# Performance work log

Hardware: AMD Instinct MI355X
Metric: run time of the kernel (lower is better)

The kernel has to match this reference:

```python
import jax, jax.numpy as jnp
import numpy as np

H, D = 8, 16
F = H * D              # hidden_dim = 128
L = 2                  # num HGT layers
NS = [50000, 20000, 10000]                     # gene, disease, drug node counts
EDGE_META = [(0, 0), (0, 1), (2, 0), (2, 1)]   # (src_type, dst_type) per edge type
ES = [300000, 150000, 100000, 50000]
OFFS = [0, NS[0], NS[0] + NS[1], NS[0] + NS[1] + NS[2]]
NTOT = OFFS[-1]
R, T = len(EDGE_META), len(NS)
SQRT_D = float(np.sqrt(D))


def setup_inputs() -> dict:
    key = jax.random.key(0)
    ks = jax.random.split(key, 32)
    inp = {}
    inp["x_gene"] = jax.random.normal(ks[0], (NS[0], F), jnp.float32)
    inp["x_disease"] = jax.random.normal(ks[1], (NS[1], F), jnp.float32)
    inp["x_drug"] = jax.random.normal(ks[2], (NS[2], F), jnp.float32)
    inp["Wkqv"] = 0.05 * jax.random.normal(ks[3], (L, T, F, 3 * F), jnp.float32)
    inp["bkqv"] = jnp.zeros((L, T, 3 * F), jnp.float32)
    inp["Ak"] = 0.1 * jax.random.normal(ks[4], (L, R, H, D, D), jnp.float32)
    inp["Av"] = 0.1 * jax.random.normal(ks[5], (L, R, H, D, D), jnp.float32)
    inp["prel"] = jnp.ones((L, R, H), jnp.float32)   # PyG inits p_rel to ones
    inp["Wout"] = 0.05 * jax.random.normal(ks[6], (L, T, F, F), jnp.float32)
    inp["bout"] = jnp.zeros((L, T, F), jnp.float32)
    inp["skip"] = jnp.ones((L, T), jnp.float32)      # PyG inits skip to 1
    names = ["ei_gg", "ei_gd", "ei_rg", "ei_rd"]
    for i, (name, (st, dt), E) in enumerate(zip(names, EDGE_META, ES)):
        src = jax.random.randint(ks[10 + 2 * i], (E,), 0, NS[st], dtype=jnp.int32)
        dst = jax.random.randint(ks[11 + 2 * i], (E,), 0, NS[dt], dtype=jnp.int32)
        inp[name] = jnp.stack([src, dst])
    return inp


def _hgt_layer(xs, eis, Wkqv_l, bkqv_l, Ak_l, Av_l, prel_l, Wout_l, bout_l, skip_l):
    """One PyG-style HGTConv layer over the heterogeneous graph."""
    kqv = [x @ Wkqv_l[t] + bkqv_l[t] for t, x in enumerate(xs)]
    k = [a[:, :F].reshape(-1, H, D) for a in kqv]
    q = [a[:, F:2 * F].reshape(-1, H, D) for a in kqv]
    v = [a[:, 2 * F:].reshape(-1, H, D) for a in kqv]

    alphas, dsts, ves = [], [], []
    for r, (st, dt) in enumerate(EDGE_META):
        src, dst = eis[r][0], eis[r][1]
        # relation-specific per-head transforms applied on source node set
        k_r = jnp.einsum('nhd,hde->nhe', k[st], Ak_l[r])
        v_r = jnp.einsum('nhd,hde->nhe', v[st], Av_l[r])
        ke = k_r[src]                      # [E, H, D]
        ve = v_r[src]                      # [E, H, D]
        qe = q[dt][dst]                    # [E, H, D]
        a = (qe * ke).sum(-1) * prel_l[r] / SQRT_D   # [E, H]
        alphas.append(a)
        dsts.append(dst + OFFS[dt])
        ves.append(ve)
    alpha = jnp.concatenate(alphas, 0)     # [Etot, H]
    dstg = jnp.concatenate(dsts, 0)        # [Etot]
    ve = jnp.concatenate(ves, 0)           # [Etot, H, D]

    # segment softmax over all incoming edges per destination node
    amax = jax.ops.segment_max(alpha, dstg, num_segments=NTOT)
    ex = jnp.exp(alpha - amax[dstg])
    denom = jax.ops.segment_sum(ex, dstg, num_segments=NTOT)
    w = ex / denom[dstg]
    out = jax.ops.segment_sum(ve * w[..., None], dstg, num_segments=NTOT)
    out = out.reshape(NTOT, F)

    new_xs = []
    for t, x in enumerate(xs):
        o_t = out[OFFS[t]:OFFS[t + 1]]
        o = jax.nn.gelu(o_t, approximate=False) @ Wout_l[t] + bout_l[t]
        a_s = jax.nn.sigmoid(skip_l[t])
        new_xs.append(a_s * o + (1.0 - a_s) * x)
    return new_xs


def reference(x_gene, x_disease, x_drug, Wkqv, bkqv, Ak, Av, prel, Wout, bout,
              skip, ei_gg, ei_gd, ei_rg, ei_rd):
    xs = [x_gene, x_disease, x_drug]
    eis = [ei_gg, ei_gd, ei_rg, ei_rd]
    for l in range(L):
        new = _hgt_layer(xs, eis, Wkqv[l], bkqv[l], Ak[l], Av[l], prel[l],
                         Wout[l], bout[l], skip[l])
        # encoder: dropout(relu(conv_out)) + residual; dropout = identity (eval)
        xs = [jax.nn.relu(n) + x for n, x in zip(new, xs)]
    return tuple(xs)
```

## Files before the change

### kernel.cpp

```cpp
#include <hip/hip_runtime.h>


#define NTOT  80000
#define ETOT  600000
#define NSRC  120000

typedef unsigned short u16;
typedef unsigned int   u32;
typedef __attribute__((ext_vector_type(8))) short short8;
typedef __attribute__((ext_vector_type(4))) float f32x4;

__device__ __forceinline__ float bf2f(u16 u){
  union { u32 i; float f; } v; v.i = ((u32)u) << 16; return v.f;
}
__device__ __forceinline__ u16 f2bf(float f){
  union { float f; u32 i; } v; v.f = f;
  u32 x = v.i;
  return (u16)((x + 0x7fffu + ((x >> 16) & 1u)) >> 16);
}
__device__ __forceinline__ void unp4(uint4 a, float* o){
  union { u32 i; float f; } t;
  t.i = a.x << 16;        o[0]=t.f;  t.i = a.x & 0xffff0000u; o[1]=t.f;
  t.i = a.y << 16;        o[2]=t.f;  t.i = a.y & 0xffff0000u; o[3]=t.f;
  t.i = a.z << 16;        o[4]=t.f;  t.i = a.z & 0xffff0000u; o[5]=t.f;
  t.i = a.w << 16;        o[6]=t.f;  t.i = a.w & 0xffff0000u; o[7]=t.f;
}
__device__ __forceinline__ void load16bf(const u16* p, float* o){
  unp4(*(const uint4*)p, o); unp4(*(const uint4*)(p + 8), o + 8);
}


__global__ __launch_bounds__(256) void copy_init(
    const float* __restrict__ xg, const float* __restrict__ xd,
    const float* __restrict__ xr, float* __restrict__ X, u16* __restrict__ Xbf)
{
  int i = blockIdx.x * 256 + threadIdx.x;
  if (i >= 2560000) return;
  const float* src; int off;
  if (i < 1600000)      { src = xg; off = i; }
  else if (i < 2240000) { src = xd; off = i - 1600000; }
  else                  { src = xr; off = i - 2240000; }
  float4 v = ((const float4*)src)[off];
  ((float4*)X)[i] = v;
  uint2 b;
  b.x = (u32)f2bf(v.x) | ((u32)f2bf(v.y) << 16);
  b.y = (u32)f2bf(v.z) | ((u32)f2bf(v.w) << 16);
  ((uint2*)Xbf)[i] = b;
}

__global__ __launch_bounds__(256) void zero_cc(int* __restrict__ cnt, int* __restrict__ cur){
  int i = blockIdx.x * 256 + threadIdx.x;
  if (i < NTOT){ cnt[i] = 0; cur[i] = 0; }
}


__global__ __launch_bounds__(256) void count_all(
    const int* __restrict__ e0, const int* __restrict__ e1,
    const int* __restrict__ e2, const int* __restrict__ e3,
    int* __restrict__ cnt)
{
  int e = blockIdx.x * 256 + threadIdx.x;
  if (e >= ETOT) return;
  const int* ei; int E, loc, offd;
  if (e < 300000)      { ei = e0; E = 300000; loc = e;          offd = 0; }
  else if (e < 450000) { ei = e1; E = 150000; loc = e - 300000; offd = 50000; }
  else if (e < 550000) { ei = e2; E = 100000; loc = e - 450000; offd = 0; }
  else                 { ei = e3; E = 50000;  loc = e - 550000; offd = 50000; }
  atomicAdd(&cnt[offd + ei[E + loc]], 1);
}

__global__ __launch_bounds__(256) void scan_partial(const int* __restrict__ cnt,
                             int* __restrict__ rowp, int* __restrict__ bsum){
  __shared__ int s[256];
  int tid = threadIdx.x;
  int i = blockIdx.x * 256 + tid;
  int v = (i < NTOT) ? cnt[i] : 0;
  s[tid] = v; __syncthreads();
  for (int off = 1; off < 256; off <<= 1){
    int t = (tid >= off) ? s[tid - off] : 0;
    __syncthreads();
    s[tid] += t;
    __syncthreads();
  }
  if (i < NTOT) rowp[i] = s[tid] - v;
  if (tid == 255) bsum[blockIdx.x] = s[255];
}

__global__ __launch_bounds__(256) void scan_block(int* __restrict__ bsum, int nb){
  __shared__ int b[512];
  __shared__ int p[256];
  int tid = threadIdx.x;
  b[tid]       = (tid < nb)       ? bsum[tid]       : 0;
  b[tid + 256] = (tid + 256 < nb) ? bsum[tid + 256] : 0;
  __syncthreads();
  int pv = b[2*tid] + b[2*tid + 1];
  p[tid] = pv; __syncthreads();
  for (int off = 1; off < 256; off <<= 1){
    int t = (tid >= off) ? p[tid - off] : 0;
    __syncthreads();
    p[tid] += t;
    __syncthreads();
  }
  int excl = p[tid] - pv;
  int e0 = excl, e1 = excl + b[2*tid];
  __syncthreads();
  if (2*tid < nb)   bsum[2*tid]     = e0;
  if (2*tid+1 < nb) bsum[2*tid + 1] = e1;
}

__global__ __launch_bounds__(256) void scan_add(int* __restrict__ rowp, const int* __restrict__ bsum){
  int i = blockIdx.x * 256 + threadIdx.x;
  if (i < NTOT) rowp[i] += bsum[i >> 8];
}

__global__ __launch_bounds__(256) void scatter_all(
    const int* __restrict__ e0, const int* __restrict__ e1,
    const int* __restrict__ e2, const int* __restrict__ e3,
    const int* __restrict__ rowp, int* __restrict__ cur,
    int* __restrict__ elist)
{
  int e = blockIdx.x * 256 + threadIdx.x;
  if (e >= ETOT) return;
  const int* ei; int E, loc, offd, rnoff, rel;
  if (e < 300000)      { ei = e0; E = 300000; loc = e;          offd = 0;     rnoff = 0;      rel = 0; }
  else if (e < 450000) { ei = e1; E = 150000; loc = e - 300000; offd = 50000; rnoff = 50000;  rel = 1; }
  else if (e < 550000) { ei = e2; E = 100000; loc = e - 450000; offd = 0;     rnoff = 100000; rel = 2; }
  else                 { ei = e3; E = 50000;  loc = e - 550000; offd = 50000; rnoff = 110000; rel = 3; }
  int src = ei[loc], dst = ei[E + loc];
  int dstg = offd + dst;
  int pos = atomicAdd(&cur[dstg], 1);
  elist[rowp[dstg] + pos] = ((rnoff + src) << 2) | rel;
}


__global__ __launch_bounds__(256) void build_wefft(
    const float* __restrict__ Wkqv, const float* __restrict__ Ak,
    const float* __restrict__ Av, u16* __restrict__ WeffT)
{
  int i = blockIdx.x * 256 + threadIdx.x;
  if (i >= 8*32768) return;
  int lr = i >> 15, rem = i & 32767, n = rem >> 7, k = rem & 127;
  int l = lr >> 2, r = lr & 3;
  int st = (r >= 2) ? 2 : 0;
  const float* W = Wkqv + (size_t)(l*3 + st) * 49152;
  float acc = 0.f;
  if (n < 128){
    int h = n >> 4, e = n & 15;
    const float* Am = Ak + (size_t)(l*4 + r) * 2048 + h*256;
#pragma unroll
    for (int d = 0; d < 16; d++) acc += W[k*384 + h*16 + d] * Am[d*16 + e];
  } else {
    int n2 = n - 128, h = n2 >> 4, e = n2 & 15;
    const float* Am = Av + (size_t)(l*4 + r) * 2048 + h*256;
#pragma unroll
    for (int d = 0; d < 16; d++) acc += W[k*384 + 256 + h*16 + d] * Am[d*16 + e];
  }
  WeffT[i] = f2bf(acc);
}

__global__ __launch_bounds__(256) void build_beff(
    const float* __restrict__ bkqv, const float* __restrict__ Ak,
    const float* __restrict__ Av, float* __restrict__ beff)
{
  int lr = blockIdx.x;
  int l = lr >> 2, r = lr & 3;
  int st = (r >= 2) ? 2 : 0;
  int j = threadIdx.x;
  const float* b = bkqv + (size_t)(l*3 + st) * 384;
  float acc = 0.f;
  if (j < 128){
    int h = j >> 4, e = j & 15;
    const float* Am = Ak + (size_t)(l*4 + r) * 2048 + h*256;
#pragma unroll
    for (int d = 0; d < 16; d++) acc += b[h*16 + d] * Am[d*16 + e];
  } else {
    int j2 = j - 128, h = j2 >> 4, e = j2 & 15;
    const float* Am = Av + (size_t)(l*4 + r) * 2048 + h*256;
#pragma unroll
    for (int d = 0; d < 16; d++) acc += b[256 + h*16 + d] * Am[d*16 + e];
  }
  beff[lr * 256 + j] = acc;
}


__global__ __launch_bounds__(256) void conv_w(
    const float* __restrict__ Wkqv, const float* __restrict__ Wout,
    u16* __restrict__ WqT, u16* __restrict__ WoutT)
{
  int i = blockIdx.x * 256 + threadIdx.x;
  if (i >= 2*6*16384) return;
  if (i < 6*16384){
    int lt = i >> 14, rem = i & 16383, n = rem >> 7, k = rem & 127;
    WqT[i] = f2bf(Wkqv[(size_t)lt*49152 + k*384 + 128 + n]);
  } else {
    int j = i - 6*16384;
    int lt = j >> 14, rem = j & 16383, n = rem >> 7, k = rem & 127;
    WoutT[j] = f2bf(Wout[(size_t)lt*16384 + k*128 + n]);
  }
}


__device__ __forceinline__ void stage_bt(const u16* __restrict__ src, u16* BTl){
  int tid = threadIdx.x;
  const uint4* g = (const uint4*)src;
  uint4 tmp[8];
#pragma unroll
  for (int i = 0; i < 8; i++) tmp[i] = g[tid + i*256];
#pragma unroll
  for (int i = 0; i < 8; i++){
    int L = (tid + i*256) * 16;
    int Ls = L ^ (((L >> 8) & 7) << 4);
    *(uint4*)((char*)BTl + Ls) = tmp[i];
  }
  __syncthreads();
}

__device__ __forceinline__ void gemm_core(
    const u16* __restrict__ A, const u16* BTl, int M, int bm,
    f32x4 acc[8][2])
{
  int tid = threadIdx.x;
  int lane = tid & 63, w = tid >> 6;
  int quad = lane >> 4, lm = lane & 15;
  short8 af[2][4];
#pragma unroll
  for (int mf = 0; mf < 2; mf++){
    int row = bm + w*32 + mf*16 + lm;
    if (row < M){
      const u16* ap = A + (size_t)row*128 + quad*8;
#pragma unroll
      for (int c = 0; c < 4; c++) af[mf][c] = *(const short8*)(ap + c*32);
    } else {
      short8 z = {0,0,0,0,0,0,0,0};
#pragma unroll
      for (int c = 0; c < 4; c++) af[mf][c] = z;
    }
  }
#pragma unroll
  for (int nt = 0; nt < 8; nt++)
#pragma unroll
    for (int mf = 0; mf < 2; mf++) acc[nt][mf] = (f32x4){0.f,0.f,0.f,0.f};
#pragma unroll
  for (int nt = 0; nt < 8; nt++){
    int rowb = nt*16 + lm;
    int base = rowb*256 + quad*16;
    int sw = (rowb & 7) << 4;
#pragma unroll
    for (int c = 0; c < 4; c++){
      short8 bf = *(const short8*)((const char*)BTl + ((base + c*64) ^ sw));
      acc[nt][0] = __builtin_amdgcn_mfma_f32_16x16x32_bf16(af[0][c], bf, acc[nt][0], 0, 0, 0);
      acc[nt][1] = __builtin_amdgcn_mfma_f32_16x16x32_bf16(af[1][c], bf, acc[nt][1], 0, 0, 0);
    }
  }
}

__global__ __launch_bounds__(256) void mfma_gemm_q(
    const u16* __restrict__ Xbf, const u16* __restrict__ WqTl,
    const float* __restrict__ bl, u16* __restrict__ qg)
{
  __shared__ u16 BTl[16384];
  int by = blockIdx.x;
  int t, bm, M, roff;
  if (by < 391)      { t = 0; bm = by*128;        M = 50000; roff = 0; }
  else if (by < 548) { t = 1; bm = (by-391)*128;  M = 20000; roff = 50000; }
  else               { t = 2; bm = (by-548)*128;  M = 10000; roff = 70000; }
  stage_bt(WqTl + (size_t)t*16384, BTl);
  const u16* A = Xbf + (size_t)roff*128;
  const float* bias = bl + (size_t)t*384 + 128;
  u16* C = qg + (size_t)roff*128;
  f32x4 acc[8][2];
  gemm_core(A, BTl, M, bm, acc);
  int lane = threadIdx.x & 63, w = threadIdx.x >> 6;
  int quad = lane >> 4, lm = lane & 15;
#pragma unroll
  for (int nt = 0; nt < 8; nt++){
    int col = nt*16 + lm;
    float bb = bias[col];
#pragma unroll
    for (int mf = 0; mf < 2; mf++)
#pragma unroll
      for (int i = 0; i < 4; i++){
        int r = bm + w*32 + mf*16 + quad*4 + i;
        if (r < M) C[(size_t)r*128 + col] = f2bf(acc[nt][mf][i] + bb);
      }
  }
}

__global__ __launch_bounds__(256) void mfma_gemm_kv(
    const u16* __restrict__ Xbf, const u16* __restrict__ WeffTl,
    const float* __restrict__ beffl, u16* __restrict__ kv)
{
  __shared__ u16 BTl[16384];
  int by = blockIdx.y;
  int r, bm, M, soff, ooff;
  if (by < 391)      { r = 0; bm = by*128;        M = 50000; soff = 0;     ooff = 0; }
  else if (by < 782) { r = 1; bm = (by-391)*128;  M = 50000; soff = 0;     ooff = 50000; }
  else if (by < 861) { r = 2; bm = (by-782)*128;  M = 10000; soff = 70000; ooff = 100000; }
  else               { r = 3; bm = (by-861)*128;  M = 10000; soff = 70000; ooff = 110000; }
  int bn = blockIdx.x * 128;
  stage_bt(WeffTl + (size_t)r*32768 + (size_t)bn*128, BTl);
  const u16* A = Xbf + (size_t)soff*128;
  const float* bias = beffl + (size_t)r*256;
  u16* C = kv + (size_t)ooff*256;
  f32x4 acc[8][2];
  gemm_core(A, BTl, M, bm, acc);
  int lane = threadIdx.x & 63, w = threadIdx.x >> 6;
  int quad = lane >> 4, lm = lane & 15;
#pragma unroll
  for (int nt = 0; nt < 8; nt++){
    int col = bn + nt*16 + lm;
    float bb = bias[col];
#pragma unroll
    for (int mf = 0; mf < 2; mf++)
#pragma unroll
      for (int i = 0; i < 4; i++){
        int r2 = bm + w*32 + mf*16 + quad*4 + i;
        if (r2 < M) C[(size_t)r2*256 + col] = f2bf(acc[nt][mf][i] + bb);
      }
  }
}

__global__ __launch_bounds__(256) void mfma_gemm_out(
    const u16* __restrict__ Gall, const u16* __restrict__ WoutTl,
    const float* __restrict__ bl, const float* __restrict__ skipl,
    float* __restrict__ Xall, u16* __restrict__ Xbfall)
{
  __shared__ u16 BTl[16384];
  int by = blockIdx.x;
  int t, bm, M, roff;
  if (by < 391)      { t = 0; bm = by*128;        M = 50000; roff = 0; }
  else if (by < 548) { t = 1; bm = (by-391)*128;  M = 20000; roff = 50000; }
  else               { t = 2; bm = (by-548)*128;  M = 10000; roff = 70000; }
  stage_bt(WoutTl + (size_t)t*16384, BTl);
  const u16* A = Gall + (size_t)roff*128;
  const float* bias = bl + (size_t)t*128;
  float* X = Xall + (size_t)roff*128;
  u16* Xb = Xbfall + (size_t)roff*128;
  f32x4 acc[8][2];
  gemm_core(A, BTl, M, bm, acc);
  float a_s = 1.f / (1.f + expf(-skipl[t]));
  float b_s = 1.f - a_s;
  int lane = threadIdx.x & 63, w = threadIdx.x >> 6;
  int quad = lane >> 4, lm = lane & 15;
#pragma unroll
  for (int nt = 0; nt < 8; nt++){
    int col = nt*16 + lm;
    float bb = bias[col];
#pragma unroll
    for (int mf = 0; mf < 2; mf++)
#pragma unroll
      for (int i = 0; i < 4; i++){
        int r = bm + w*32 + mf*16 + quad*4 + i;
        if (r < M){
          float* xp = X + (size_t)r*128 + col;
          float x = *xp;
          float o = acc[nt][mf][i] + bb;
          float xn = fmaxf(a_s*o + b_s*x, 0.f) + x;
          *xp = xn;
          Xb[(size_t)r*128 + col] = f2bf(xn);
        }
      }
  }
}


__global__ __launch_bounds__(256) void attn_kernel(
    u16* __restrict__ qg,
    const u16* __restrict__ kv,
    const float* __restrict__ prel,
    const int* __restrict__ rowp, const int* __restrict__ cnt,
    const int* __restrict__ elist)
{
  int gid = blockIdx.x * 256 + threadIdx.x;
  int n = gid >> 4;
  if (n >= NTOT) return;
  int lane = threadIdx.x & 63;
  int sub = (lane >> 3) & 1;
  int h = lane & 7;
  float sc0 = prel[0*8+h]*0.25f, sc1 = prel[1*8+h]*0.25f,
        sc2 = prel[2*8+h]*0.25f, sc3 = prel[3*8+h]*0.25f;
  float q[16];
  load16bf(qg + (size_t)n * 128 + h*16, q);
  float acc[16] = {};
  float dsum = 0.f;
  int start = rowp[n], c = cnt[n];

  auto edge = [&](int ev, uint4 ka, uint4 kb, uint4 va, uint4 vb){
    float ke[16], ve[16];
    unp4(ka, ke); unp4(kb, ke + 8);
    unp4(va, ve); unp4(vb, ve + 8);
    float a = 0.f;
#pragma unroll
    for (int d = 0; d < 16; d++) a += q[d] * ke[d];
    int r = ev & 3;
    float s = (r == 0) ? sc0 : (r == 1) ? sc1 : (r == 2) ? sc2 : sc3;
    float ex = expf(a * s);
    dsum += ex;
#pragma unroll
    for (int d = 0; d < 16; d++) acc[d] += ex * ve[d];
  };

  int idx = sub;
#pragma unroll 1
  for (; idx + 6 < c; idx += 8){
    int e0 = elist[start + idx + 0], e1 = elist[start + idx + 2],
        e2 = elist[start + idx + 4], e3 = elist[start + idx + 6];
    const u16* p0 = kv + (size_t)(e0 >> 2) * 256 + h*16;
    const u16* p1 = kv + (size_t)(e1 >> 2) * 256 + h*16;
    const u16* p2 = kv + (size_t)(e2 >> 2) * 256 + h*16;
    const u16* p3 = kv + (size_t)(e3 >> 2) * 256 + h*16;
    uint4 k0a = *(const uint4*)p0,         k0b = *(const uint4*)(p0 + 8);
    uint4 k1a = *(const uint4*)p1,         k1b = *(const uint4*)(p1 + 8);
    uint4 k2a = *(const uint4*)p2,         k2b = *(const uint4*)(p2 + 8);
    uint4 k3a = *(const uint4*)p3,         k3b = *(const uint4*)(p3 + 8);
    uint4 v0a = *(const uint4*)(p0 + 128), v0b = *(const uint4*)(p0 + 136);
    uint4 v1a = *(const uint4*)(p1 + 128), v1b = *(const uint4*)(p1 + 136);
    uint4 v2a = *(const uint4*)(p2 + 128), v2b = *(const uint4*)(p2 + 136);
    uint4 v3a = *(const uint4*)(p3 + 128), v3b = *(const uint4*)(p3 + 136);
    edge(e0, k0a, k0b, v0a, v0b);
    edge(e1, k1a, k1b, v1a, v1b);
    edge(e2, k2a, k2b, v2a, v2b);
    edge(e3, k3a, k3b, v3a, v3b);
  }
#pragma unroll 1
  for (; idx < c; idx += 2){
    int ev = elist[start + idx];
    const u16* p = kv + (size_t)(ev >> 2) * 256 + h*16;
    uint4 ka = *(const uint4*)p,         kb = *(const uint4*)(p + 8);
    uint4 va = *(const uint4*)(p + 128), vb = *(const uint4*)(p + 136);
    edge(ev, ka, kb, va, vb);
  }

  dsum += __shfl_xor(dsum, 8);
#pragma unroll
  for (int d = 0; d < 16; d++) acc[d] += __shfl_xor(acc[d], 8);

  if (sub == 0){
    float inv = (c > 0) ? 1.f / dsum : 0.f;
    u16 o[16];
#pragma unroll
    for (int d = 0; d < 16; d++){
      float x = acc[d] * inv;
      o[d] = f2bf(0.5f * x * (1.f + erff(x * 0.70710678118654752f)));
    }
    uint4 p0, p1;
    p0.x = o[0]|(o[1]<<16);   p0.y = o[2]|(o[3]<<16);
    p0.z = o[4]|(o[5]<<16);   p0.w = o[6]|(o[7]<<16);
    p1.x = o[8]|(o[9]<<16);   p1.y = o[10]|(o[11]<<16);
    p1.z = o[12]|(o[13]<<16); p1.w = o[14]|(o[15]<<16);
    u16* op = qg + (size_t)n * 128 + h*16;
    *(uint4*)op = p0; *(uint4*)(op + 8) = p1;
  }
}


extern "C" void kernel_launch(void* const* d_in, const int* in_sizes, int n_in,
                              void* d_out, int out_size, void* d_ws, size_t ws_size,
                              hipStream_t stream)
{
  const float* xg   = (const float*)d_in[0];
  const float* xd   = (const float*)d_in[1];
  const float* xr_  = (const float*)d_in[2];
  const float* Wkqv = (const float*)d_in[3];
  const float* bkqv = (const float*)d_in[4];
  const float* Ak   = (const float*)d_in[5];
  const float* Av   = (const float*)d_in[6];
  const float* prel = (const float*)d_in[7];
  const float* Wout = (const float*)d_in[8];
  const float* bout = (const float*)d_in[9];
  const float* skip = (const float*)d_in[10];
  const int* ei[4] = {(const int*)d_in[11], (const int*)d_in[12],
                      (const int*)d_in[13], (const int*)d_in[14]};

  float* X = (float*)d_out;

  char* p = (char*)d_ws;
  auto alloc = [&](size_t b)->void*{ void* r = (void*)p; p += (b + 255) & ~(size_t)255; return r; };
  int*   cnt   = (int*)  alloc((size_t)NTOT * 4);
  int*   rowp  = (int*)  alloc((size_t)NTOT * 4);
  int*   cur   = (int*)  alloc((size_t)NTOT * 4);
  int*   bsum  = (int*)  alloc(512 * 4);
  int*   elist = (int*)  alloc((size_t)ETOT * 4);
  float* beff  = (float*)alloc((size_t)8 * 256 * 4);
  u16*   qg    = (u16*)  alloc((size_t)NTOT * 128 * 2);
  u16*   kv    = (u16*)  alloc((size_t)NSRC * 256 * 2);
  u16*   Xbf   = (u16*)  alloc((size_t)NTOT * 128 * 2);
  u16*   WqT   = (u16*)  alloc((size_t)6 * 16384 * 2);
  u16*   WeffT = (u16*)  alloc((size_t)8 * 32768 * 2);
  u16*   WoutT = (u16*)  alloc((size_t)6 * 16384 * 2);
  (void)ws_size; (void)in_sizes; (void)n_in; (void)out_size;

  copy_init<<<10000, 256, 0, stream>>>(xg, xd, xr_, X, Xbf);
  zero_cc<<<313, 256, 0, stream>>>(cnt, cur);

  count_all<<<(ETOT+255)/256, 256, 0, stream>>>(ei[0], ei[1], ei[2], ei[3], cnt);
  scan_partial<<<313, 256, 0, stream>>>(cnt, rowp, bsum);
  scan_block<<<1, 256, 0, stream>>>(bsum, 313);
  scan_add<<<313, 256, 0, stream>>>(rowp, bsum);
  scatter_all<<<(ETOT+255)/256, 256, 0, stream>>>(ei[0], ei[1], ei[2], ei[3], rowp, cur, elist);

  build_wefft<<<1024, 256, 0, stream>>>(Wkqv, Ak, Av, WeffT);
  build_beff<<<8, 256, 0, stream>>>(bkqv, Ak, Av, beff);
  conv_w<<<768, 256, 0, stream>>>(Wkqv, Wout, WqT, WoutT);

  for (int l = 0; l < 2; l++){
    mfma_gemm_q<<<627, 256, 0, stream>>>(
        Xbf, WqT + (size_t)l*3*16384, bkqv + (size_t)l*3*384, qg);
    mfma_gemm_kv<<<dim3(2, 940), 256, 0, stream>>>(
        Xbf, WeffT + (size_t)l*4*32768, beff + (size_t)l*4*256, kv);
    attn_kernel<<<5000, 256, 0, stream>>>(qg, kv, prel + l*32, rowp, cnt, elist);
    mfma_gemm_out<<<627, 256, 0, stream>>>(
        qg, WoutT + (size_t)l*3*16384, bout + (size_t)l*3*128, skip + l*3, X, Xbf);
  }
}
```

Before: 467.8 us.

## Merge Q and KV GEMMs into one launch, halve M-tile, fuse setup kernels

Combines the Q projection GEMM and the relation-specific K/V GEMM into a single kernel dispatched over a flat block index. The per-block M tile drops from 128 to 64 rows, so each wave handles one 16-row fragment, and the output GEMM gets the same tile size. The init/zero kernels and the three weight-preparation kernels are each merged into one launch. The aim is to cut launch count and improve occupancy and tail balance. The cost is twice as many blocks, each restaging the 32KB B tile into LDS, so there is less B reuse per staging.

```diff
diff --git a/kernel.cpp b/kernel.cpp
--- a/kernel.cpp
+++ b/kernel.cpp
@@ -30,27 +30,27 @@
 }
 
 
-__global__ __launch_bounds__(256) void copy_init(
+__global__ __launch_bounds__(256) void init_all(
     const float* __restrict__ xg, const float* __restrict__ xd,
-    const float* __restrict__ xr, float* __restrict__ X, u16* __restrict__ Xbf)
+    const float* __restrict__ xr, float* __restrict__ X, u16* __restrict__ Xbf,
+    int* __restrict__ cnt, int* __restrict__ cur)
 {
   int i = blockIdx.x * 256 + threadIdx.x;
-  if (i >= 2560000) return;
-  const float* src; int off;
-  if (i < 1600000)      { src = xg; off = i; }
-  else if (i < 2240000) { src = xd; off = i - 1600000; }
-  else                  { src = xr; off = i - 2240000; }
-  float4 v = ((const float4*)src)[off];
-  ((float4*)X)[i] = v;
-  uint2 b;
-  b.x = (u32)f2bf(v.x) | ((u32)f2bf(v.y) << 16);
-  b.y = (u32)f2bf(v.z) | ((u32)f2bf(v.w) << 16);
-  ((uint2*)Xbf)[i] = b;
-}
-
-__global__ __launch_bounds__(256) void zero_cc(int* __restrict__ cnt, int* __restrict__ cur){
-  int i = blockIdx.x * 256 + threadIdx.x;
-  if (i < NTOT){ cnt[i] = 0; cur[i] = 0; }
+  if (i < 2560000){
+    const float* src; int off;
+    if (i < 1600000)      { src = xg; off = i; }
+    else if (i < 2240000) { src = xd; off = i - 1600000; }
+    else                  { src = xr; off = i - 2240000; }
+    float4 v = ((const float4*)src)[off];
+    ((float4*)X)[i] = v;
+    uint2 b;
+    b.x = (u32)f2bf(v.x) | ((u32)f2bf(v.y) << 16);
+    b.y = (u32)f2bf(v.z) | ((u32)f2bf(v.w) << 16);
+    ((uint2*)Xbf)[i] = b;
+  } else {
+    int j = i - 2560000;
+    if (j < NTOT){ cnt[j] = 0; cur[j] = 0; }
+  }
 }
 
 
@@ -133,70 +133,65 @@
 }
 
 
-__global__ __launch_bounds__(256) void build_wefft(
-    const float* __restrict__ Wkqv, const float* __restrict__ Ak,
-    const float* __restrict__ Av, u16* __restrict__ WeffT)
+__global__ __launch_bounds__(256) void wprep_all(
+    const float* __restrict__ Wkqv, const float* __restrict__ bkqv,
+    const float* __restrict__ Ak, const float* __restrict__ Av,
+    const float* __restrict__ Wout,
+    u16* __restrict__ WeffT, u16* __restrict__ WqT, u16* __restrict__ WoutT,
+    float* __restrict__ beff)
 {
   int i = blockIdx.x * 256 + threadIdx.x;
-  if (i >= 8*32768) return;
-  int lr = i >> 15, rem = i & 32767, n = rem >> 7, k = rem & 127;
+  if (i < 8*32768){
+    int lr = i >> 15, rem = i & 32767, n = rem >> 7, k = rem & 127;
+    int l = lr >> 2, r = lr & 3;
+    int st = (r >= 2) ? 2 : 0;
+    const float* W = Wkqv + (size_t)(l*3 + st) * 49152;
+    float acc = 0.f;
+    if (n < 128){
+      int h = n >> 4, e = n & 15;
+      const float* Am = Ak + (size_t)(l*4 + r) * 2048 + h*256;
+#pragma unroll
+      for (int d = 0; d < 16; d++) acc += W[k*384 + h*16 + d] * Am[d*16 + e];
+    } else {
+      int n2 = n - 128, h = n2 >> 4, e = n2 & 15;
+      const float* Am = Av + (size_t)(l*4 + r) * 2048 + h*256;
+#pragma unroll
+      for (int d = 0; d < 16; d++) acc += W[k*384 + 256 + h*16 + d] * Am[d*16 + e];
+    }
+    WeffT[i] = f2bf(acc);
+    return;
+  }
+  int j = i - 8*32768;
+  if (j < 2*6*16384){
+    if (j < 6*16384){
+      int lt = j >> 14, rem = j & 16383, n = rem >> 7, k = rem & 127;
+      WqT[j] = f2bf(Wkqv[(size_t)lt*49152 + k*384 + 128 + n]);
+    } else {
+      int j2 = j - 6*16384;
+      int lt = j2 >> 14, rem = j2 & 16383, n = rem >> 7, k = rem & 127;
+      WoutT[j2] = f2bf(Wout[(size_t)lt*16384 + k*128 + n]);
+    }
+    return;
+  }
+  int m = j - 2*6*16384;
+  if (m >= 2048) return;
+  int lr = m >> 8, jj = m & 255;
   int l = lr >> 2, r = lr & 3;
   int st = (r >= 2) ? 2 : 0;
-  const float* W = Wkqv + (size_t)(l*3 + st) * 49152;
-  float acc = 0.f;
-  if (n < 128){
-    int h = n >> 4, e = n & 15;
-    const float* Am = Ak + (size_t)(l*4 + r) * 2048 + h*256;
-#pragma unroll
-    for (int d = 0; d < 16; d++) acc += W[k*384 + h*16 + d] * Am[d*16 + e];
-  } else {
-    int n2 = n - 128, h = n2 >> 4, e = n2 & 15;
-    const float* Am = Av + (size_t)(l*4 + r) * 2048 + h*256;
-#pragma unroll
-    for (int d = 0; d < 16; d++) acc += W[k*384 + 256 + h*16 + d] * Am[d*16 + e];
-  }
-  WeffT[i] = f2bf(acc);
-}
-
-__global__ __launch_bounds__(256) void build_beff(
-    const float* __restrict__ bkqv, const float* __restrict__ Ak,
-    const float* __restrict__ Av, float* __restrict__ beff)
-{
-  int lr = blockIdx.x;
-  int l = lr >> 2, r = lr & 3;
-  int st = (r >= 2) ? 2 : 0;
-  int j = threadIdx.x;
   const float* b = bkqv + (size_t)(l*3 + st) * 384;
   float acc = 0.f;
-  if (j < 128){
-    int h = j >> 4, e = j & 15;
+  if (jj < 128){
+    int h = jj >> 4, e = jj & 15;
     const float* Am = Ak + (size_t)(l*4 + r) * 2048 + h*256;
 #pragma unroll
     for (int d = 0; d < 16; d++) acc += b[h*16 + d] * Am[d*16 + e];
   } else {
-    int j2 = j - 128, h = j2 >> 4, e = j2 & 15;
+    int j2 = jj - 128, h = j2 >> 4, e = j2 & 15;
     const float* Am = Av + (size_t)(l*4 + r) * 2048 + h*256;
 #pragma unroll
     for (int d = 0; d < 16; d++) acc += b[256 + h*16 + d] * Am[d*16 + e];
   }
-  beff[lr * 256 + j] = acc;
-}
-
-
-__global__ __launch_bounds__(256) void conv_w(
-    const float* __restrict__ Wkqv, const float* __restrict__ Wout,
-    u16* __restrict__ WqT, u16* __restrict__ WoutT)
-{
-  int i = blockIdx.x * 256 + threadIdx.x;
-  if (i >= 2*6*16384) return;
-  if (i < 6*16384){
-    int lt = i >> 14, rem = i & 16383, n = rem >> 7, k = rem & 127;
-    WqT[i] = f2bf(Wkqv[(size_t)lt*49152 + k*384 + 128 + n]);
-  } else {
-    int j = i - 6*16384;
-    int lt = j >> 14, rem = j & 16383, n = rem >> 7, k = rem & 127;
-    WoutT[j] = f2bf(Wout[(size_t)lt*16384 + k*128 + n]);
-  }
+  beff[lr * 256 + jj] = acc;
 }
 
 
@@ -215,31 +210,26 @@
   __syncthreads();
 }
 
-__device__ __forceinline__ void gemm_core(
+__device__ __forceinline__ void gemm_core16(
     const u16* __restrict__ A, const u16* BTl, int M, int bm,
-    f32x4 acc[8][2])
+    f32x4 acc[8])
 {
   int tid = threadIdx.x;
   int lane = tid & 63, w = tid >> 6;
   int quad = lane >> 4, lm = lane & 15;
-  short8 af[2][4];
-#pragma unroll
-  for (int mf = 0; mf < 2; mf++){
-    int row = bm + w*32 + mf*16 + lm;
-    if (row < M){
-      const u16* ap = A + (size_t)row*128 + quad*8;
-#pragma unroll
-      for (int c = 0; c < 4; c++) af[mf][c] = *(const short8*)(ap + c*32);
-    } else {
-      short8 z = {0,0,0,0,0,0,0,0};
-#pragma unroll
-      for (int c = 0; c < 4; c++) af[mf][c] = z;
-    }
-  }
-#pragma unroll
-  for (int nt = 0; nt < 8; nt++)
-#pragma unroll
-    for (int mf = 0; mf < 2; mf++) acc[nt][mf] = (f32x4){0.f,0.f,0.f,0.f};
+  int row = bm + w*16 + lm;
+  short8 af[4];
+  if (row < M){
+    const u16* ap = A + (size_t)row*128 + quad*8;
+#pragma unroll
+    for (int c = 0; c < 4; c++) af[c] = *(const short8*)(ap + c*32);
+  } else {
+    short8 z = {0,0,0,0,0,0,0,0};
+#pragma unroll
+    for (int c = 0; c < 4; c++) af[c] = z;
+  }
+#pragma unroll
+  for (int nt = 0; nt < 8; nt++) acc[nt] = (f32x4){0.f,0.f,0.f,0.f};
 #pragma unroll
   for (int nt = 0; nt < 8; nt++){
     int rowb = nt*16 + lm;
@@ -248,28 +238,47 @@
 #pragma unroll
     for (int c = 0; c < 4; c++){
       short8 bf = *(const short8*)((const char*)BTl + ((base + c*64) ^ sw));
-      acc[nt][0] = __builtin_amdgcn_mfma_f32_16x16x32_bf16(af[0][c], bf, acc[nt][0], 0, 0, 0);
-      acc[nt][1] = __builtin_amdgcn_mfma_f32_16x16x32_bf16(af[1][c], bf, acc[nt][1], 0, 0, 0);
-    }
-  }
-}
-
-__global__ __launch_bounds__(256) void mfma_gemm_q(
-    const u16* __restrict__ Xbf, const u16* __restrict__ WqTl,
-    const float* __restrict__ bl, u16* __restrict__ qg)
+      acc[nt] = __builtin_amdgcn_mfma_f32_16x16x32_bf16(af[c], bf, acc[nt], 0, 0, 0);
+    }
+  }
+}
+
+__global__ __launch_bounds__(256) void mfma_gemm_qkv(
+    const u16* __restrict__ Xbf,
+    const u16* __restrict__ WqTl, const float* __restrict__ bl,
+    const u16* __restrict__ WeffTl, const float* __restrict__ beffl,
+    u16* __restrict__ qg, u16* __restrict__ kv)
 {
   __shared__ u16 BTl[16384];
   int by = blockIdx.x;
-  int t, bm, M, roff;
-  if (by < 391)      { t = 0; bm = by*128;        M = 50000; roff = 0; }
-  else if (by < 548) { t = 1; bm = (by-391)*128;  M = 20000; roff = 50000; }
-  else               { t = 2; bm = (by-548)*128;  M = 10000; roff = 70000; }
-  stage_bt(WqTl + (size_t)t*16384, BTl);
-  const u16* A = Xbf + (size_t)roff*128;
-  const float* bias = bl + (size_t)t*384 + 128;
-  u16* C = qg + (size_t)roff*128;
-  f32x4 acc[8][2];
-  gemm_core(A, BTl, M, bm, acc);
+  const u16* A; const u16* BT; const float* bias;
+  u16* C; int ldc, bm, M, bn;
+  if (by < 1252){
+    int t, roff;
+    if (by < 782)       { t = 0; bm = by*64;         M = 50000; roff = 0; }
+    else if (by < 1095) { t = 1; bm = (by-782)*64;   M = 20000; roff = 50000; }
+    else                { t = 2; bm = (by-1095)*64;  M = 10000; roff = 70000; }
+    A = Xbf + (size_t)roff*128;
+    BT = WqTl + (size_t)t*16384;
+    bias = bl + (size_t)t*384 + 128;
+    C = qg + (size_t)roff*128; ldc = 128; bn = 0;
+  } else {
+    int idx = by - 1252;
+    bn = (idx < 1878) ? 0 : 128;
+    int tile = (idx < 1878) ? idx : idx - 1878;
+    int r, soff, ooff;
+    if (tile < 782)       { r = 0; bm = tile*64;        M = 50000; soff = 0;     ooff = 0; }
+    else if (tile < 1564) { r = 1; bm = (tile-782)*64;  M = 50000; soff = 0;     ooff = 50000; }
+    else if (tile < 1721) { r = 2; bm = (tile-1564)*64; M = 10000; soff = 70000; ooff = 100000; }
+    else                  { r = 3; bm = (tile-1721)*64; M = 10000; soff = 70000; ooff = 110000; }
+    A = Xbf + (size_t)soff*128;
+    BT = WeffTl + (size_t)r*32768 + (size_t)bn*128;
+    bias = beffl + (size_t)r*256 + bn;
+    C = kv + (size_t)ooff*256 + bn; ldc = 256;
+  }
+  stage_bt(BT, BTl);
+  f32x4 acc[8];
+  gemm_core16(A, BTl, M, bm, acc);
   int lane = threadIdx.x & 63, w = threadIdx.x >> 6;
   int quad = lane >> 4, lm = lane & 15;
 #pragma unroll
@@ -277,46 +286,10 @@
     int col = nt*16 + lm;
     float bb = bias[col];
 #pragma unroll
-    for (int mf = 0; mf < 2; mf++)
-#pragma unroll
-      for (int i = 0; i < 4; i++){
-        int r = bm + w*32 + mf*16 + quad*4 + i;
-        if (r < M) C[(size_t)r*128 + col] = f2bf(acc[nt][mf][i] + bb);
-      }
-  }
-}
-
-__global__ __launch_bounds__(256) void mfma_gemm_kv(
-    const u16* __restrict__ Xbf, const u16* __restrict__ WeffTl,
-    const float* __restrict__ beffl, u16* __restrict__ kv)
-{
-  __shared__ u16 BTl[16384];
-  int by = blockIdx.y;
-  int r, bm, M, soff, ooff;
-  if (by < 391)      { r = 0; bm = by*128;        M = 50000; soff = 0;     ooff = 0; }
-  else if (by < 782) { r = 1; bm = (by-391)*128;  M = 50000; soff = 0;     ooff = 50000; }
-  else if (by < 861) { r = 2; bm = (by-782)*128;  M = 10000; soff = 70000; ooff = 100000; }
-  else               { r = 3; bm = (by-861)*128;  M = 10000; soff = 70000; ooff = 110000; }
-  int bn = blockIdx.x * 128;
-  stage_bt(WeffTl + (size_t)r*32768 + (size_t)bn*128, BTl);
-  const u16* A = Xbf + (size_t)soff*128;
-  const float* bias = beffl + (size_t)r*256;
-  u16* C = kv + (size_t)ooff*256;
-  f32x4 acc[8][2];
-  gemm_core(A, BTl, M, bm, acc);
-  int lane = threadIdx.x & 63, w = threadIdx.x >> 6;
-  int quad = lane >> 4, lm = lane & 15;
-#pragma unroll
-  for (int nt = 0; nt < 8; nt++){
-    int col = bn + nt*16 + lm;
-    float bb = bias[col];
-#pragma unroll
-    for (int mf = 0; mf < 2; mf++)
-#pragma unroll
-      for (int i = 0; i < 4; i++){
-        int r2 = bm + w*32 + mf*16 + quad*4 + i;
-        if (r2 < M) C[(size_t)r2*256 + col] = f2bf(acc[nt][mf][i] + bb);
-      }
+    for (int i = 0; i < 4; i++){
+      int r = bm + w*16 + quad*4 + i;
+      if (r < M) C[(size_t)r*ldc + col] = f2bf(acc[nt][i] + bb);
+    }
   }
 }
 
@@ -328,16 +301,16 @@
   __shared__ u16 BTl[16384];
   int by = blockIdx.x;
   int t, bm, M, roff;
-  if (by < 391)      { t = 0; bm = by*128;        M = 50000; roff = 0; }
-  else if (by < 548) { t = 1; bm = (by-391)*128;  M = 20000; roff = 50000; }
-  else               { t = 2; bm = (by-548)*128;  M = 10000; roff = 70000; }
+  if (by < 782)       { t = 0; bm = by*64;         M = 50000; roff = 0; }
+  else if (by < 1095) { t = 1; bm = (by-782)*64;   M = 20000; roff = 50000; }
+  else                { t = 2; bm = (by-1095)*64;  M = 10000; roff = 70000; }
   stage_bt(WoutTl + (size_t)t*16384, BTl);
   const u16* A = Gall + (size_t)roff*128;
   const float* bias = bl + (size_t)t*128;
   float* X = Xall + (size_t)roff*128;
   u16* Xb = Xbfall + (size_t)roff*128;
-  f32x4 acc[8][2];
-  gemm_core(A, BTl, M, bm, acc);
+  f32x4 acc[8];
+  gemm_core16(A, BTl, M, bm, acc);
   float a_s = 1.f / (1.f + expf(-skipl[t]));
   float b_s = 1.f - a_s;
   int lane = threadIdx.x & 63, w = threadIdx.x >> 6;
@@ -347,19 +320,17 @@
     int col = nt*16 + lm;
     float bb = bias[col];
 #pragma unroll
-    for (int mf = 0; mf < 2; mf++)
-#pragma unroll
-      for (int i = 0; i < 4; i++){
-        int r = bm + w*32 + mf*16 + quad*4 + i;
-        if (r < M){
-          float* xp = X + (size_t)r*128 + col;
-          float x = *xp;
-          float o = acc[nt][mf][i] + bb;
-          float xn = fmaxf(a_s*o + b_s*x, 0.f) + x;
-          *xp = xn;
-          Xb[(size_t)r*128 + col] = f2bf(xn);
-        }
+    for (int i = 0; i < 4; i++){
+      int r = bm + w*16 + quad*4 + i;
+      if (r < M){
+        float* xp = X + (size_t)r*128 + col;
+        float x = *xp;
+        float o = acc[nt][i] + bb;
+        float xn = fmaxf(a_s*o + b_s*x, 0.f) + x;
+        *xp = xn;
+        Xb[(size_t)r*128 + col] = f2bf(xn);
       }
+    }
   }
 }
 
@@ -490,8 +461,7 @@
   u16*   WoutT = (u16*)  alloc((size_t)6 * 16384 * 2);
   (void)ws_size; (void)in_sizes; (void)n_in; (void)out_size;
 
-  copy_init<<<10000, 256, 0, stream>>>(xg, xd, xr_, X, Xbf);
-  zero_cc<<<313, 256, 0, stream>>>(cnt, cur);
+  init_all<<<(2560000+NTOT+255)/256, 256, 0, stream>>>(xg, xd, xr_, X, Xbf, cnt, cur);
 
   count_all<<<(ETOT+255)/256, 256, 0, stream>>>(ei[0], ei[1], ei[2], ei[3], cnt);
   scan_partial<<<313, 256, 0, stream>>>(cnt, rowp, bsum);
@@ -499,17 +469,17 @@
   scan_add<<<313, 256, 0, stream>>>(rowp, bsum);
   scatter_all<<<(ETOT+255)/256, 256, 0, stream>>>(ei[0], ei[1], ei[2], ei[3], rowp, cur, elist);
 
-  build_wefft<<<1024, 256, 0, stream>>>(Wkqv, Ak, Av, WeffT);
-  build_beff<<<8, 256, 0, stream>>>(bkqv, Ak, Av, beff);
-  conv_w<<<768, 256, 0, stream>>>(Wkqv, Wout, WqT, WoutT);
+  wprep_all<<<(8*32768 + 2*6*16384 + 2048 + 255)/256, 256, 0, stream>>>(
+      Wkqv, bkqv, Ak, Av, Wout, WeffT, WqT, WoutT, beff);
 
   for (int l = 0; l < 2; l++){
-    mfma_gemm_q<<<627, 256, 0, stream>>>(
-        Xbf, WqT + (size_t)l*3*16384, bkqv + (size_t)l*3*384, qg);
-    mfma_gemm_kv<<<dim3(2, 940), 256, 0, stream>>>(
-        Xbf, WeffT + (size_t)l*4*32768, beff + (size_t)l*4*256, kv);
+    mfma_gemm_qkv<<<1252 + 3756, 256, 0, stream>>>(
+        Xbf,
+        WqT + (size_t)l*3*16384, bkqv + (size_t)l*3*384,
+        WeffT + (size_t)l*4*32768, beff + (size_t)l*4*256,
+        qg, kv);
     attn_kernel<<<5000, 256, 0, stream>>>(qg, kv, prel + l*32, rowp, cnt, elist);
-    mfma_gemm_out<<<627, 256, 0, stream>>>(
+    mfma_gemm_out<<<1252, 256, 0, stream>>>(
         qg, WoutT + (size_t)l*3*16384, bout + (size_t)l*3*128, skip + l*3, X, Xbf);
   }
 }
```

After: 454.8 us. -2.8%, faster.
